# Performance work log

Measured on AMD Instinct MI355X. Metric: run time of the kernel, lower is better.

Reference implementation:

```python
import jax, jax.numpy as jnp
import numpy as np

TEMPERATURE = 8.0  # sqrt(d_head=64)

def setup_inputs() -> dict:
    key = jax.random.key(0)
    kq, kk, kv = jax.random.split(key, 3)
    shape = (2, 16, 2048, 64)  # [B, H, S, D]
    q = jax.random.normal(kq, shape, dtype=jnp.float32)
    k = jax.random.normal(kk, shape, dtype=jnp.float32)
    v = jax.random.normal(kv, shape, dtype=jnp.float32)
    return {"q": q, "k": k, "v": v}

def reference(q, k, v):
    # attn = softmax((q / temperature) @ k^T) ; dropout is identity in eval
    scores = jnp.einsum('bhqd,bhkd->bhqk', q / TEMPERATURE, k)  # [B,H,S,S]
    attn = jax.nn.softmax(scores, axis=-1)
    out = jnp.einsum('bhqk,bhkd->bhqd', attn, v)  # [B,H,S,D]
    return out
```

## Files before the change

### kernel.cpp

```cpp
#include <hip/hip_runtime.h>
#include <hip/hip_bf16.h>

typedef __bf16 bf16_t;
typedef bf16_t bf16x4 __attribute__((ext_vector_type(4)));
typedef bf16_t bf16x8 __attribute__((ext_vector_type(8)));
typedef float f32x4 __attribute__((ext_vector_type(4)));

#define S_LEN 2048
#define HD 64
#define NT 32
#define BHN 32
#define QSCALE 0.18033688f

__device__ __forceinline__ void gload16(const bf16_t* g, void* l) {
    __builtin_amdgcn_global_load_lds(
        (const __attribute__((address_space(1))) void*)g,
        (__attribute__((address_space(3))) void*)l, 16, 0, 0);
}

__global__ __launch_bounds__(256)
void prep_kv(const float* __restrict__ kg, const float* __restrict__ vg,
             bf16_t* __restrict__ kb, bf16_t* __restrict__ vtb) {
    __shared__ bf16_t Vl[64 * 68];
    const int tid = threadIdx.x;
    const int kt0 = blockIdx.x * 64;
    const int bh  = blockIdx.y;
    const size_t gbase = (size_t)bh * S_LEN * HD;
    #pragma unroll
    for (int j = 0; j < 4; ++j) {
        int idx = j * 256 + tid;
        int key = idx >> 4;
        int d0  = (idx & 15) * 4;
        const f32x4 k4 = *(const f32x4*)(kg + gbase + (size_t)(kt0 + key) * HD + d0);
        const f32x4 v4 = *(const f32x4*)(vg + gbase + (size_t)(kt0 + key) * HD + d0);
        bf16x4 kbv, vbv;
        #pragma unroll
        for (int e = 0; e < 4; ++e) { kbv[e] = (bf16_t)k4[e]; vbv[e] = (bf16_t)v4[e]; }
        *(bf16x4*)(kb + gbase + (size_t)(kt0 + key) * HD + d0) = kbv;
        *(bf16x4*)&Vl[key * 68 + d0] = vbv;
    }
    __syncthreads();
    const int d   = tid >> 2;
    const int q16 = tid & 3;
    const int kp  = q16 >> 1, h = q16 & 1;
    bf16_t* orow = vtb + (size_t)bh * HD * S_LEN + (size_t)d * S_LEN + kt0;
    #pragma unroll
    for (int gg = 0; gg < 4; ++gg) {
        bf16x4 o;
        #pragma unroll
        for (int r = 0; r < 4; ++r) o[r] = Vl[(q16 * 16 + gg * 4 + r) * 68 + d];
        *(bf16x4*)(orow + kp * 32 + gg * 8 + h * 4) = o;
    }
}

__global__ __launch_bounds__(128, 2)
void attn_fwd_bf16(const float* __restrict__ qg, const bf16_t* __restrict__ kb,
                   const bf16_t* __restrict__ vtb, float* __restrict__ og) {
    __shared__ __align__(16) char lds[32768];

    const int tid  = threadIdx.x;
    const int wave = tid >> 6;
    const int lane = tid & 63;
    const int g    = lane >> 4;
    const int ln   = lane & 15;

    const int fid  = blockIdx.x;
    const int bid2 = (fid & 7) * 128 + (fid >> 3);
    const int bh   = bid2 >> 5;
    const int qt   = bid2 & 31;
    const int qrow0 = qt * 64 + wave * 32;
    const size_t base = (size_t)bh * S_LEN * HD;

    bf16x8 qf[2][2];
    #pragma unroll
    for (int qg2 = 0; qg2 < 2; ++qg2) {
        const float* qp = qg + base + (size_t)(qrow0 + qg2 * 16 + ln) * HD;
        #pragma unroll
        for (int c = 0; c < 2; ++c)
            #pragma unroll
            for (int i = 0; i < 8; ++i)
                qf[qg2][c][i] = (bf16_t)(qp[c * 32 + g * 8 + i] * QSCALE);
    }
    asm volatile("s_waitcnt vmcnt(0)" ::: "memory");

    bf16x8 ones;
    #pragma unroll
    for (int i = 0; i < 8; ++i) ones[i] = (bf16_t)1.0f;

    const int r0 = tid >> 3, s0 = tid & 7;
    const bf16_t* ks = kb  + base + r0 * HD + (s0 ^ (r0 & 7)) * 8;
    const bf16_t* vs = vtb + base + (size_t)r0 * S_LEN + (s0 ^ (r0 & 7)) * 8;
    char* ldb = lds + tid * 16;

#define STAGE(kt, b) do { \
        _Pragma("unroll") \
        for (int i = 0; i < 4; ++i) \
            gload16(ks + (size_t)(kt) * 4096 + i * 16 * HD, ldb + (b) * 8192 + i * 2048); \
        _Pragma("unroll") \
        for (int i = 0; i < 4; ++i) \
            gload16(vs + (kt) * 64 + (size_t)i * 16 * S_LEN, ldb + 16384 + (b) * 8192 + i * 2048); \
    } while (0)

    int kof[4][2], voff[4][2];
    #pragma unroll
    for (int kt2 = 0; kt2 < 4; ++kt2)
        #pragma unroll
        for (int c = 0; c < 2; ++c)
            kof[kt2][c] = (kt2 * 16 + ln) * 128 + (((c << 2) + g) ^ (ln & 7)) * 16;
    #pragma unroll
    for (int t = 0; t < 4; ++t)
        #pragma unroll
        for (int kp = 0; kp < 2; ++kp)
            voff[t][kp] = 16384 + (t * 16 + ln) * 128 + (((kp << 2) + g) ^ (ln & 7)) * 16;

    f32x4 acc[2][4];
    f32x4 accl[2];
    #pragma unroll
    for (int qg2 = 0; qg2 < 2; ++qg2) {
        accl[qg2] = f32x4{0.f, 0.f, 0.f, 0.f};
        #pragma unroll
        for (int t = 0; t < 4; ++t) acc[qg2][t] = f32x4{0.f, 0.f, 0.f, 0.f};
    }

    STAGE(0, 0);

    for (int kt = 0; kt < NT; ++kt) {
        asm volatile("s_waitcnt vmcnt(0)" ::: "memory");
        asm volatile("s_barrier" ::: "memory");
        if (kt + 1 < NT) STAGE(kt + 1, (kt + 1) & 1);
        const char* kbr = lds + (kt & 1) * 8192;
        const char* vbr = kbr;

        f32x4 sv01[2][2];
        #pragma unroll
        for (int kt2 = 0; kt2 < 2; ++kt2) {
            const bf16x8 kf0 = *(const bf16x8*)(kbr + kof[kt2][0]);
            const bf16x8 kf1 = *(const bf16x8*)(kbr + kof[kt2][1]);
            #pragma unroll
            for (int qg2 = 0; qg2 < 2; ++qg2) {
                f32x4 s = f32x4{0.f, 0.f, 0.f, 0.f};
                s = __builtin_amdgcn_mfma_f32_16x16x32_bf16(kf0, qf[qg2][0], s, 0, 0, 0);
                s = __builtin_amdgcn_mfma_f32_16x16x32_bf16(kf1, qf[qg2][1], s, 0, 0, 0);
                sv01[kt2][qg2] = s;
            }
        }

        bf16x8 pa0[2];
        #pragma unroll
        for (int qg2 = 0; qg2 < 2; ++qg2)
            #pragma unroll
            for (int i = 0; i < 8; ++i)
                pa0[qg2][i] = (bf16_t)__builtin_amdgcn_exp2f(sv01[i >> 2][qg2][i & 3]);

        f32x4 sv23[2][2];
        #pragma unroll
        for (int kt2 = 0; kt2 < 2; ++kt2) {
            const bf16x8 kf0 = *(const bf16x8*)(kbr + kof[2 + kt2][0]);
            const bf16x8 kf1 = *(const bf16x8*)(kbr + kof[2 + kt2][1]);
            #pragma unroll
            for (int qg2 = 0; qg2 < 2; ++qg2) {
                f32x4 s = f32x4{0.f, 0.f, 0.f, 0.f};
                s = __builtin_amdgcn_mfma_f32_16x16x32_bf16(kf0, qf[qg2][0], s, 0, 0, 0);
                s = __builtin_amdgcn_mfma_f32_16x16x32_bf16(kf1, qf[qg2][1], s, 0, 0, 0);
                sv23[kt2][qg2] = s;
            }
        }

        #pragma unroll
        for (int t = 0; t < 4; ++t) {
            const bf16x8 vf0 = *(const bf16x8*)(vbr + voff[t][0]);
            #pragma unroll
            for (int qg2 = 0; qg2 < 2; ++qg2)
                acc[qg2][t] = __builtin_amdgcn_mfma_f32_16x16x32_bf16(pa0[qg2], vf0, acc[qg2][t], 0, 0, 0);
        }

        bf16x8 pa1[2];
        #pragma unroll
        for (int qg2 = 0; qg2 < 2; ++qg2)
            #pragma unroll
            for (int i = 0; i < 8; ++i)
                pa1[qg2][i] = (bf16_t)__builtin_amdgcn_exp2f(sv23[i >> 2][qg2][i & 3]);

        #pragma unroll
        for (int t = 0; t < 4; ++t) {
            const bf16x8 vf1 = *(const bf16x8*)(vbr + voff[t][1]);
            #pragma unroll
            for (int qg2 = 0; qg2 < 2; ++qg2)
                acc[qg2][t] = __builtin_amdgcn_mfma_f32_16x16x32_bf16(pa1[qg2], vf1, acc[qg2][t], 0, 0, 0);
        }

        #pragma unroll
        for (int qg2 = 0; qg2 < 2; ++qg2) {
            accl[qg2] = __builtin_amdgcn_mfma_f32_16x16x32_bf16(pa0[qg2], ones, accl[qg2], 0, 0, 0);
            accl[qg2] = __builtin_amdgcn_mfma_f32_16x16x32_bf16(pa1[qg2], ones, accl[qg2], 0, 0, 0);
        }
    }
#undef STAGE

    #pragma unroll
    for (int qg2 = 0; qg2 < 2; ++qg2) {
        float* ob = og + base + (size_t)(qrow0 + qg2 * 16) * HD;
        float il[4];
        #pragma unroll
        for (int r = 0; r < 4; ++r) il[r] = 1.f / accl[qg2][r];
        #pragma unroll
        for (int t = 0; t < 4; ++t)
            #pragma unroll
            for (int r = 0; r < 4; ++r)
                ob[(size_t)(4 * g + r) * HD + t * 16 + ln] = acc[qg2][t][r] * il[r];
    }
}

#define LDP 72
__global__ __launch_bounds__(256, 2)
void attn_fwd_fallback(const float* __restrict__ qg, const float* __restrict__ kg,
                       const float* __restrict__ vg, float* __restrict__ og) {
    __shared__ __align__(16) bf16_t Kl[64 * LDP];
    __shared__ __align__(16) bf16_t Vt[HD * LDP];
    const int tid = threadIdx.x, wave = tid >> 6, lane = tid & 63;
    const int g = lane >> 4, ln = lane & 15;
    const int bh = blockIdx.y, qrow0 = blockIdx.x * 64 + wave * 16;
    const size_t base = (size_t)bh * S_LEN * HD;
    bf16x8 qf[2];
    {
        const float* qp = qg + base + (size_t)(qrow0 + ln) * HD;
        #pragma unroll
        for (int c = 0; c < 2; ++c)
            #pragma unroll
            for (int i = 0; i < 8; ++i) qf[c][i] = (bf16_t)(qp[c * 32 + g * 8 + i] * 0.125f);
    }
    f32x4 acc[4];
    #pragma unroll
    for (int t = 0; t < 4; ++t) acc[t] = f32x4{0.f, 0.f, 0.f, 0.f};
    float m_run = -3e38f, l_run = 0.f;
    const float* kbase = kg + base;
    const float* vbase = vg + base;
    const int vkb = (tid & 15) * 4, vdb = (tid >> 4) * 4;
    for (int kt = 0; kt < NT; ++kt) {
        __syncthreads();
        #pragma unroll
        for (int j = 0; j < 4; ++j) {
            int idx = j * 256 + tid, key = idx >> 4, d0 = (idx & 15) * 4;
            const f32x4 k4 = *(const f32x4*)(kbase + (size_t)(kt * 64 + key) * HD + d0);
            bf16x4 kbv;
            #pragma unroll
            for (int e = 0; e < 4; ++e) kbv[e] = (bf16_t)k4[e];
            *(bf16x4*)&Kl[key * LDP + d0] = kbv;
        }
        {
            f32x4 v4[4];
            #pragma unroll
            for (int e = 0; e < 4; ++e)
                v4[e] = *(const f32x4*)(vbase + (size_t)(kt * 64 + vkb + e) * HD + vdb);
            #pragma unroll
            for (int j = 0; j < 4; ++j) {
                bf16x4 vb;
                #pragma unroll
                for (int e = 0; e < 4; ++e) vb[e] = (bf16_t)v4[e][j];
                *(bf16x4*)&Vt[(vdb + j) * LDP + vkb] = vb;
            }
        }
        __syncthreads();
        float p[4][4];
        float mx = -3e38f;
        #pragma unroll
        for (int kt2 = 0; kt2 < 4; ++kt2) {
            f32x4 sx = f32x4{0.f, 0.f, 0.f, 0.f};
            #pragma unroll
            for (int c = 0; c < 2; ++c) {
                const bf16x8 kf = *(const bf16x8*)&Kl[(kt2 * 16 + ln) * LDP + c * 32 + g * 8];
                sx = __builtin_amdgcn_mfma_f32_16x16x32_bf16(kf, qf[c], sx, 0, 0, 0);
            }
            #pragma unroll
            for (int rr = 0; rr < 4; ++rr) { p[kt2][rr] = sx[rr]; mx = fmaxf(mx, sx[rr]); }
        }
        mx = fmaxf(mx, __shfl_xor(mx, 16, 64));
        mx = fmaxf(mx, __shfl_xor(mx, 32, 64));
        const float mnew = fmaxf(m_run, mx);
        const float scale = __expf(m_run - mnew);
        m_run = mnew;
        float rs = 0.f;
        #pragma unroll
        for (int kt2 = 0; kt2 < 4; ++kt2)
            #pragma unroll
            for (int rr = 0; rr < 4; ++rr) {
                const float e = __expf(p[kt2][rr] - mnew);
                p[kt2][rr] = e; rs += e;
            }
        rs += __shfl_xor(rs, 16, 64);
        rs += __shfl_xor(rs, 32, 64);
        l_run = l_run * scale + rs;
        float sc[4];
        #pragma unroll
        for (int rr = 0; rr < 4; ++rr) sc[rr] = __shfl(scale, 4 * g + rr, 64);
        #pragma unroll
        for (int t = 0; t < 4; ++t)
            #pragma unroll
            for (int rr = 0; rr < 4; ++rr) acc[t][rr] *= sc[rr];
        bf16x8 pa[2];
        #pragma unroll
        for (int kp = 0; kp < 2; ++kp)
            #pragma unroll
            for (int i = 0; i < 8; ++i) pa[kp][i] = (bf16_t)p[2 * kp + (i >> 2)][i & 3];
        #pragma unroll
        for (int t = 0; t < 4; ++t)
            #pragma unroll
            for (int kp = 0; kp < 2; ++kp) {
                const bf16_t* vrow = &Vt[(t * 16 + ln) * LDP + 32 * kp + 4 * g];
                const bf16x4 lo = *(const bf16x4*)(vrow);
                const bf16x4 hi = *(const bf16x4*)(vrow + 16);
                bf16x8 vf;
                #pragma unroll
                for (int e = 0; e < 4; ++e) { vf[e] = lo[e]; vf[4 + e] = hi[e]; }
                acc[t] = __builtin_amdgcn_mfma_f32_16x16x32_bf16(pa[kp], vf, acc[t], 0, 0, 0);
            }
    }
    const float invl = 1.f / l_run;
    float il[4];
    #pragma unroll
    for (int rr = 0; rr < 4; ++rr) il[rr] = __shfl(invl, 4 * g + rr, 64);
    float* ob = og + base + (size_t)qrow0 * HD;
    #pragma unroll
    for (int t = 0; t < 4; ++t)
        #pragma unroll
        for (int rr = 0; rr < 4; ++rr)
            ob[(size_t)(4 * g + rr) * HD + t * 16 + ln] = acc[t][rr] * il[rr];
}

extern "C" void kernel_launch(void* const* d_in, const int* in_sizes, int n_in,
                              void* d_out, int out_size, void* d_ws, size_t ws_size,
                              hipStream_t stream) {
    const float* q = (const float*)d_in[0];
    const float* k = (const float*)d_in[1];
    const float* v = (const float*)d_in[2];
    float* out = (float*)d_out;
    const int bh = in_sizes[0] / (S_LEN * HD);
    const size_t plane = (size_t)bh * S_LEN * HD;
    const size_t need  = 2 * plane * sizeof(bf16_t);

    if (bh == BHN && ws_size >= need) {
        bf16_t* kb  = (bf16_t*)d_ws;
        bf16_t* vtb = kb + plane;
        prep_kv<<<dim3(NT, bh), 256, 0, stream>>>(k, v, kb, vtb);
        attn_fwd_bf16<<<dim3(bh * 32), 128, 0, stream>>>(q, kb, vtb, out);
    } else {
        attn_fwd_fallback<<<dim3(S_LEN / 64, bh), 256, 0, stream>>>(q, k, v, out);
    }
}
```

Before: 56.74 us.

## Grow attention blocks to 8 waves sharing each staged K/V tile

Measured after the change: 50.73 us. -10.6%, faster.

```diff
diff --git a/kernel.cpp b/kernel.cpp
--- a/kernel.cpp
+++ b/kernel.cpp
@@ -53,7 +53,7 @@
     }
 }
 
-__global__ __launch_bounds__(128, 2)
+__global__ __launch_bounds__(512, 1)
 void attn_fwd_bf16(const float* __restrict__ qg, const bf16_t* __restrict__ kb,
                    const bf16_t* __restrict__ vtb, float* __restrict__ og) {
     __shared__ __align__(16) char lds[32768];
@@ -65,10 +65,10 @@
     const int ln   = lane & 15;
 
     const int fid  = blockIdx.x;
-    const int bid2 = (fid & 7) * 128 + (fid >> 3);
-    const int bh   = bid2 >> 5;
-    const int qt   = bid2 & 31;
-    const int qrow0 = qt * 64 + wave * 32;
+    const int bid2 = (fid & 7) * 32 + (fid >> 3);
+    const int bh   = bid2 >> 3;
+    const int qt   = bid2 & 7;
+    const int qrow0 = qt * 256 + wave * 32;
     const size_t base = (size_t)bh * S_LEN * HD;
 
     bf16x8 qf[2][2];
@@ -87,18 +87,14 @@
     #pragma unroll
     for (int i = 0; i < 8; ++i) ones[i] = (bf16_t)1.0f;
 
-    const int r0 = tid >> 3, s0 = tid & 7;
-    const bf16_t* ks = kb  + base + r0 * HD + (s0 ^ (r0 & 7)) * 8;
-    const bf16_t* vs = vtb + base + (size_t)r0 * S_LEN + (s0 ^ (r0 & 7)) * 8;
+    const int r = tid >> 3, s = tid & 7;
+    const bf16_t* ks = kb  + base + r * HD + (s ^ (r & 7)) * 8;
+    const bf16_t* vs = vtb + base + (size_t)r * S_LEN + (s ^ (r & 7)) * 8;
     char* ldb = lds + tid * 16;
 
 #define STAGE(kt, b) do { \
-        _Pragma("unroll") \
-        for (int i = 0; i < 4; ++i) \
-            gload16(ks + (size_t)(kt) * 4096 + i * 16 * HD, ldb + (b) * 8192 + i * 2048); \
-        _Pragma("unroll") \
-        for (int i = 0; i < 4; ++i) \
-            gload16(vs + (kt) * 64 + (size_t)i * 16 * S_LEN, ldb + 16384 + (b) * 8192 + i * 2048); \
+        gload16(ks + (size_t)(kt) * 4096, ldb + (b) * 8192); \
+        gload16(vs + (kt) * 64, ldb + 16384 + (b) * 8192); \
     } while (0)
 
     int kof[4][2], voff[4][2];
@@ -138,10 +134,10 @@
             const bf16x8 kf1 = *(const bf16x8*)(kbr + kof[kt2][1]);
             #pragma unroll
             for (int qg2 = 0; qg2 < 2; ++qg2) {
-                f32x4 s = f32x4{0.f, 0.f, 0.f, 0.f};
-                s = __builtin_amdgcn_mfma_f32_16x16x32_bf16(kf0, qf[qg2][0], s, 0, 0, 0);
-                s = __builtin_amdgcn_mfma_f32_16x16x32_bf16(kf1, qf[qg2][1], s, 0, 0, 0);
-                sv01[kt2][qg2] = s;
+                f32x4 sx = f32x4{0.f, 0.f, 0.f, 0.f};
+                sx = __builtin_amdgcn_mfma_f32_16x16x32_bf16(kf0, qf[qg2][0], sx, 0, 0, 0);
+                sx = __builtin_amdgcn_mfma_f32_16x16x32_bf16(kf1, qf[qg2][1], sx, 0, 0, 0);
+                sv01[kt2][qg2] = sx;
             }
         }
 
@@ -159,10 +155,10 @@
             const bf16x8 kf1 = *(const bf16x8*)(kbr + kof[2 + kt2][1]);
             #pragma unroll
             for (int qg2 = 0; qg2 < 2; ++qg2) {
-                f32x4 s = f32x4{0.f, 0.f, 0.f, 0.f};
-                s = __builtin_amdgcn_mfma_f32_16x16x32_bf16(kf0, qf[qg2][0], s, 0, 0, 0);
-                s = __builtin_amdgcn_mfma_f32_16x16x32_bf16(kf1, qf[qg2][1], s, 0, 0, 0);
-                sv23[kt2][qg2] = s;
+                f32x4 sx = f32x4{0.f, 0.f, 0.f, 0.f};
+                sx = __builtin_amdgcn_mfma_f32_16x16x32_bf16(kf0, qf[qg2][0], sx, 0, 0, 0);
+                sx = __builtin_amdgcn_mfma_f32_16x16x32_bf16(kf1, qf[qg2][1], sx, 0, 0, 0);
+                sv23[kt2][qg2] = sx;
             }
         }
 
@@ -202,12 +198,12 @@
         float* ob = og + base + (size_t)(qrow0 + qg2 * 16) * HD;
         float il[4];
         #pragma unroll
-        for (int r = 0; r < 4; ++r) il[r] = 1.f / accl[qg2][r];
+        for (int rr = 0; rr < 4; ++rr) il[rr] = 1.f / accl[qg2][rr];
         #pragma unroll
         for (int t = 0; t < 4; ++t)
             #pragma unroll
-            for (int r = 0; r < 4; ++r)
-                ob[(size_t)(4 * g + r) * HD + t * 16 + ln] = acc[qg2][t][r] * il[r];
+            for (int rr = 0; rr < 4; ++rr)
+                ob[(size_t)(4 * g + rr) * HD + t * 16 + ln] = acc[qg2][t][rr] * il[rr];
     }
 }
 
@@ -342,7 +338,7 @@
         bf16_t* kb  = (bf16_t*)d_ws;
         bf16_t* vtb = kb + plane;
         prep_kv<<<dim3(NT, bh), 256, 0, stream>>>(k, v, kb, vtb);
-        attn_fwd_bf16<<<dim3(bh * 32), 128, 0, stream>>>(q, kb, vtb, out);
+        attn_fwd_bf16<<<dim3(bh * 8), 512, 0, stream>>>(q, kb, vtb, out);
     } else {
         attn_fwd_fallback<<<dim3(S_LEN / 64, bh), 256, 0, stream>>>(q, k, v, out);
     }
```
